# Optimization experiments

Hardware: AMD Instinct MI355X
Metric: run time of the kernel (lower is better)

The kernel has to match this reference:

```python
import jax, jax.numpy as jnp
import numpy as np

N_NODES = 50000
N_EDGES = 400000
DIMS = 32
HEADS = 6
FEAT = DIMS * HEADS  # 192
NEG_SLOPE = 0.2  # PyG GATv2Conv default


def glorot(key, shape):
    fan_in, fan_out = shape[0], shape[1]
    lim = jnp.sqrt(6.0 / (fan_in + fan_out))
    return jax.random.uniform(key, shape, jnp.float32, -lim, lim)


def setup_inputs() -> dict:
    key = jax.random.key(0)
    ks = jax.random.split(key, 10)
    x = jax.random.normal(ks[0], (N_NODES, FEAT), jnp.float32)
    edge_index = jax.random.randint(ks[1], (2, N_EDGES), 0, N_NODES, jnp.int32)
    edge_weights = jax.random.uniform(ks[2], (N_EDGES, 1), jnp.float32)
    W_l = glorot(ks[3], (FEAT, FEAT))   # lin_l: in -> heads*out
    b_l = jnp.zeros((FEAT,), jnp.float32)
    W_r = glorot(ks[4], (FEAT, FEAT))   # lin_r (share_weights=False)
    b_r = jnp.zeros((FEAT,), jnp.float32)
    W_edge = glorot(ks[5], (1, FEAT))   # lin_edge: edge_dim=1 -> heads*out, no bias
    att = glorot(ks[6], (HEADS, DIMS))  # attention vector per head
    bias = jnp.zeros((FEAT,), jnp.float32)
    return {"x": x, "edge_index": edge_index, "edge_weights": edge_weights,
            "W_l": W_l, "b_l": b_l, "W_r": W_r, "b_r": b_r,
            "W_edge": W_edge, "att": att, "bias": bias}


def gatv2_res(x, edge_index, edge_weights, W_l, b_l, W_r, b_r, W_edge, att, bias):
    N = x.shape[0]
    H, C = att.shape
    src0, dst0 = edge_index[0], edge_index[1]

    # add_self_loops with fill_value='mean': self-loop attr = mean of edge_attr over incoming edges
    cnt = jax.ops.segment_sum(jnp.ones((edge_weights.shape[0],), x.dtype), dst0, num_segments=N)
    loop_attr = jax.ops.segment_sum(edge_weights, dst0, num_segments=N) / jnp.maximum(cnt, 1.0)[:, None]
    loops = jnp.arange(N, dtype=src0.dtype)
    src = jnp.concatenate([src0, loops])
    dst = jnp.concatenate([dst0, loops])
    e_attr = jnp.concatenate([edge_weights, loop_attr], axis=0)  # [E+N, 1]

    x_l = (x @ W_l + b_l).reshape(N, H, C)  # source transform
    x_r = (x @ W_r + b_r).reshape(N, H, C)  # target transform
    e_emb = (e_attr @ W_edge).reshape(-1, H, C)

    # per-edge GATv2 score
    m = jax.nn.leaky_relu(x_l[src] + x_r[dst] + e_emb, NEG_SLOPE)  # [E+N, H, C]
    alpha = jnp.einsum('ehc,hc->eh', m, att)  # [E+N, H]

    # segment softmax over edges incident to each target node (self-loops guarantee coverage)
    amax = jax.lax.stop_gradient(jax.ops.segment_max(alpha, dst, num_segments=N))
    ex = jnp.exp(alpha - amax[dst])
    denom = jax.ops.segment_sum(ex, dst, num_segments=N)
    a = ex / denom[dst]  # [E+N, H]

    out = jax.ops.segment_sum(x_l[src] * a[..., None], dst, num_segments=N)  # [N, H, C]
    out = out.reshape(N, H * C) + bias

    # ResLayer: residual + ReLU (dropout = identity in eval mode)
    return jax.nn.relu(x + out)


def reference(x, edge_index, edge_weights, W_l, b_l, W_r, b_r, W_edge, att, bias):
    return gatv2_res(x, edge_index, edge_weights, W_l, b_l, W_r, b_r, W_edge, att, bias)
```

## Files before the change

kernel.cpp:

```cpp
#include <hip/hip_runtime.h>
#include <hip/hip_bf16.h>
#include <math.h>

#define N_NODES 50000
#define N_EDGES 400000
#define HEADS 6
#define DIMS 32
#define FEAT 192
#define NEG_SLOPE 0.2f

typedef __attribute__((ext_vector_type(8))) short short8;
typedef __attribute__((ext_vector_type(4))) float f32x4;

__device__ __forceinline__ unsigned short f2bu(float f) {
    __hip_bfloat16 h = __float2bfloat16(f);
    unsigned short u; __builtin_memcpy(&u, &h, 2); return u;
}
__device__ __forceinline__ float bu2f(unsigned short u) {
    return __uint_as_float(((unsigned)u) << 16);
}

#define XL_OFF    0
#define XR_OFF    19200000
#define WT_OFF    38400000
#define BLR_OFF   38547456
#define PAIR_OFF  38548992
#define DEG_OFF   41748992
#define SCAN_OFF  42148992
#define BSUM_OFF  42348992
#define BOFF_OFF  42350016
#define RANK_OFF  42351040
#define NB_SCAN ((N_NODES + 255) / 256)

__global__ __launch_bounds__(256) void k_count(const int* __restrict__ ei,
                                               int* __restrict__ deg,
                                               int* __restrict__ rank,
                                               const float* __restrict__ Wl,
                                               const float* __restrict__ Wr,
                                               const float* __restrict__ bl,
                                               const float* __restrict__ br,
                                               short* __restrict__ Wt,
                                               float* __restrict__ blr) {
    int e = blockIdx.x * blockDim.x + threadIdx.x;
    if (e < N_EDGES) rank[e] = atomicAdd(&deg[ei[N_EDGES + e]], 1);
    if (e < 384 * FEAT) {
        int n = e / FEAT, k = e - n * FEAT;
        float v = (n < FEAT) ? Wl[k * FEAT + n] : Wr[k * FEAT + (n - FEAT)];
        Wt[n * FEAT + k] = (short)f2bu(v);
    }
    if (e < 384) blr[e] = (e < FEAT) ? bl[e] : br[e - FEAT];
}

__global__ __launch_bounds__(256) void k_scan1(const int* __restrict__ deg,
                                               int* __restrict__ scan,
                                               int* __restrict__ bsums) {
    int t = threadIdx.x;
    int i = blockIdx.x * 256 + t;
    int v = (i < N_NODES) ? deg[i] : 0;
    __shared__ int s[256];
    s[t] = v; __syncthreads();
    for (int off = 1; off < 256; off <<= 1) {
        int u = (t >= off) ? s[t - off] : 0;
        __syncthreads();
        s[t] += u;
        __syncthreads();
    }
    if (i < N_NODES) scan[i] = s[t];
    if (t == 255) bsums[blockIdx.x] = s[255];
}

__global__ __launch_bounds__(256) void k_scan2(int* __restrict__ bsums,
                                               int* __restrict__ boffs) {
    int t = threadIdx.x;
    int v = (t < NB_SCAN) ? bsums[t] : 0;
    __shared__ int s[256];
    s[t] = v; __syncthreads();
    for (int off = 1; off < 256; off <<= 1) {
        int u = (t >= off) ? s[t - off] : 0;
        __syncthreads();
        s[t] += u;
        __syncthreads();
    }
    boffs[t] = s[t] - v;
}

__global__ __launch_bounds__(256) void k_fix(int* __restrict__ deg,
                                             const int* __restrict__ scan,
                                             const int* __restrict__ boffs) {
    int i = blockIdx.x * 256 + threadIdx.x;
    if (i < N_NODES) deg[i] = boffs[i >> 8] + scan[i] - deg[i];
}

#define SCAT_BLOCKS ((N_EDGES + 383) / 384)
#define GEMM_BLOCKS ((N_NODES + 63) / 64)
#define OSTRIDE 392
#define ASTRIDE 200
__global__ __launch_bounds__(384) void k_scatgemm(const int* __restrict__ ei,
                                                  const float* __restrict__ ew,
                                                  const int* __restrict__ deg,
                                                  const int* __restrict__ rank,
                                                  int2* __restrict__ pair,
                                                  const float* __restrict__ x,
                                                  const short* __restrict__ Wt,
                                                  const float* __restrict__ blr,
                                                  unsigned short* __restrict__ xl,
                                                  unsigned short* __restrict__ xr) {
    __shared__ unsigned short sOut[16 * OSTRIDE];
    __shared__ unsigned short sA[64 * ASTRIDE];
    if (blockIdx.x < SCAT_BLOCKS) {
        int e = blockIdx.x * 384 + threadIdx.x;
        if (e < N_EDGES) {
            int d = ei[N_EDGES + e];
            int slot = deg[d] + rank[e];
            int2 p; p.x = ei[e]; p.y = __float_as_int(ew[e]);
            pair[slot] = p;
        }
        return;
    }
    size_t row0 = (size_t)(blockIdx.x - SCAT_BLOCKS) * 64;

#pragma unroll
    for (int s = 0; s < 4; s++) {
        int q = threadIdx.x + s * 384;
        int row = q / 24, k0 = (q - row * 24) * 8;
        size_t gr = row0 + row;
        const float* ap = x + (gr < N_NODES ? gr : row0) * FEAT + k0;
        float4 v0 = *(const float4*)ap;
        float4 v1 = *(const float4*)(ap + 4);
        unsigned short tmp[8];
        tmp[0] = f2bu(v0.x); tmp[1] = f2bu(v0.y); tmp[2] = f2bu(v0.z); tmp[3] = f2bu(v0.w);
        tmp[4] = f2bu(v1.x); tmp[5] = f2bu(v1.y); tmp[6] = f2bu(v1.z); tmp[7] = f2bu(v1.w);
        int kw = (k0 >> 1) ^ ((row & 7) << 2);
        *(uint4*)&sA[row * ASTRIDE + kw * 2] = *(const uint4*)tmp;
    }
    __syncthreads();

    int wv   = threadIdx.x >> 6;
    int lane = threadIdx.x & 63;
    int m    = lane & 15;
    int kg   = lane >> 4;
    int ncol0 = wv * 64;

    f32x4 acc[4][4];
#pragma unroll
    for (int r = 0; r < 4; r++)
#pragma unroll
        for (int j = 0; j < 4; j++) acc[r][j] = (f32x4){0.f, 0.f, 0.f, 0.f};

#pragma unroll
    for (int ks = 0; ks < 6; ks++) {
        int kb = ks * 32 + kg * 8;
        int kw = (kb >> 1) ^ ((m & 7) << 2);
        short8 af0 = *(const short8*)&sA[m * ASTRIDE + kw * 2];
        short8 af1 = *(const short8*)&sA[(16 + m) * ASTRIDE + kw * 2];
        short8 af2 = *(const short8*)&sA[(32 + m) * ASTRIDE + kw * 2];
        short8 af3 = *(const short8*)&sA[(48 + m) * ASTRIDE + kw * 2];
        const short* wp = Wt + (size_t)(ncol0 + m) * FEAT + kb;
#pragma unroll
        for (int j = 0; j < 4; j++) {
            short8 b = *(const short8*)(wp + j * 16 * FEAT);
            acc[0][j] = __builtin_amdgcn_mfma_f32_16x16x32_bf16(af0, b, acc[0][j], 0, 0, 0);
            acc[1][j] = __builtin_amdgcn_mfma_f32_16x16x32_bf16(af1, b, acc[1][j], 0, 0, 0);
            acc[2][j] = __builtin_amdgcn_mfma_f32_16x16x32_bf16(af2, b, acc[2][j], 0, 0, 0);
            acc[3][j] = __builtin_amdgcn_mfma_f32_16x16x32_bf16(af3, b, acc[3][j], 0, 0, 0);
        }
    }

#pragma unroll
    for (int pass = 0; pass < 4; pass++) {
        if (pass) __syncthreads();
#pragma unroll
        for (int t4 = 0; t4 < 4; t4++) {
            int cc = ncol0 + t4 * 16 + m;
            float bv = blr[cc];
#pragma unroll
            for (int r = 0; r < 4; r++) {
                sOut[(kg * 4 + r) * OSTRIDE + cc] = f2bu(acc[pass][t4][r] + bv);
            }
        }
        __syncthreads();
        for (int q = threadIdx.x; q < 768; q += 384) {
            int row = q / 48, p = q - row * 48;
            size_t gr = row0 + pass * 16 + row;
            if (gr < N_NODES) {
                uint4 v = *(const uint4*)&sOut[row * OSTRIDE + p * 8];
                if (p < 24) *(uint4*)(xl + gr * FEAT + p * 8) = v;
                else        *(uint4*)(xr + gr * FEAT + (p - 24) * 8) = v;
            }
        }
    }
}

#define NPB 8
#define CEDGE 32
#define RS 100
#define APAD 36
__global__ __launch_bounds__(192) void k_node(const float* __restrict__ x,
                                              const float* __restrict__ bias,
                                              const float* __restrict__ att,
                                              const float* __restrict__ We,
                                              const int* __restrict__ scan,
                                              const int* __restrict__ boffs,
                                              const int2* __restrict__ pair,
                                              const unsigned short* __restrict__ xl,
                                              const unsigned short* __restrict__ xr,
                                              float* __restrict__ out) {
    __shared__ __align__(16) unsigned int sXL[CEDGE * RS];
    __shared__ __align__(16) unsigned int sXR[NPB * RS];
    __shared__ float sEx[CEDGE * HEADS];
    __shared__ float sExS[NPB * HEADS];
    __shared__ int   sSrc[2][CEDGE];
    __shared__ float sW[2][CEDGE];
    __shared__ int   sDst[2][CEDGE];
    __shared__ int   sStart[NPB + 1];
    __shared__ __align__(16) float sAttP[HEADS * APAD];
    __shared__ __align__(16) float sWeP[HEADS * APAD];
    __shared__ float sDen[NPB * HEADS];
    __shared__ float sWsm[NPB];

    int t = threadIdx.x;
    int h = t >> 5;
    int n0 = blockIdx.x * NPB;

    int gbase = boffs[n0 >> 8] + ((n0 & 255) ? scan[n0 - 1] : 0);
    int n8 = n0 + NPB;
    int gend = (n8 >= N_NODES) ? N_EDGES
             : (boffs[n8 >> 8] + ((n8 & 255) ? scan[n8 - 1] : 0));
    int etot = gend - gbase;
    int c0 = min(etot, CEDGE);

    if (t < c0) { int2 p = pair[gbase + t]; sSrc[0][t] = p.x; sW[0][t] = __int_as_float(p.y); }

    for (int q = t; q < HEADS * APAD; q += 192) {
        int hh = q / APAD, c = q - hh * APAD;
        if (c < 32) { sAttP[q] = att[hh * 32 + c]; sWeP[q] = We[hh * 32 + c]; }
    }
    if (t <= NPB) {
        int n = n0 + t;
        int st;
        if (n >= N_NODES) st = N_EDGES;
        else {
            int b = n >> 8;
            st = boffs[b] + ((n & 255) ? scan[n - 1] : 0);
        }
        sStart[t] = st;
    }
    if (t < NPB) {
        int n = n0 + t;
        int a = boffs[n >> 8] + ((n & 255) ? scan[n - 1] : 0);
        int n1 = n + 1;
        int b = (n1 >= N_NODES) ? N_EDGES
              : (boffs[n1 >> 8] + ((n1 & 255) ? scan[n1 - 1] : 0));
        int lo = a - gbase; if (lo < 0) lo = 0;
        int hi = b - gbase; if (hi > c0) hi = c0;
        for (int q = lo; q < hi; q++) sDst[0][q] = t;
    }
    {
        int nn = t / 24, p = t - nn * 24;
        *(uint4*)&sXR[nn * RS + p * 4] = ((const uint4*)(xr + (size_t)(n0 + nn) * FEAT))[p];
    }
    __syncthreads();

    float acc[NPB];
#pragma unroll
    for (int nn = 0; nn < NPB; nn++) acc[nn] = 0.f;
    float redR = 0.f;
    int nnD = t / HEADS, hhD = t - nnD * HEADS;

    int nch = (etot + CEDGE - 1) / CEDGE;
    for (int ci = 0; ci < nch; ci++) {
        int i0 = ci * CEDGE;
        int c  = min(etot - i0, CEDGE);
        int cn = min(etot - i0 - CEDGE, CEDGE);
        int cb = ci & 1, nb = cb ^ 1;

        {
            int nld = c * 24;
#pragma unroll
            for (int s = 0; s < 4; s++) {
                int q = t + s * 192;
                if (q < nld) {
                    int i = q / 24, p = q - i * 24;
                    *(uint4*)&sXL[i * RS + p * 4] =
                        *(const uint4*)(xl + (size_t)sSrc[cb][i] * FEAT + p * 8);
                }
            }
        }
        int2 P;
        if (t < cn) P = pair[gbase + i0 + CEDGE + t];
        if (t < NPB && cn > 0) {
            int lo = sStart[t] - gbase - i0 - CEDGE;     if (lo < 0) lo = 0;
            int hi = sStart[t + 1] - gbase - i0 - CEDGE; if (hi > cn) hi = cn;
            for (int q = lo; q < hi; q++) sDst[nb][q] = t;
        }
        __syncthreads();

        if (t < c * HEADS) {
            int i = t / HEADS, hh = t - i * HEADS;
            int nn = sDst[cb][i];
            float w = sW[cb][i];
            const uint4* pa = (const uint4*)&sXL[i * RS + hh * 16];
            const uint4* pb = (const uint4*)&sXR[nn * RS + hh * 16];
            float alpha0 = 0.f, alpha1 = 0.f;
#pragma unroll
            for (int g = 0; g < 4; g++) {
                uint4 a4 = pa[g];
                uint4 b4 = pb[g];
                float4 we0 = *(const float4*)&sWeP[hh * APAD + g * 8];
                float4 we1 = *(const float4*)&sWeP[hh * APAD + g * 8 + 4];
                float4 at0 = *(const float4*)&sAttP[hh * APAD + g * 8];
                float4 at1 = *(const float4*)&sAttP[hh * APAD + g * 8 + 4];
                float wec[8] = {we0.x, we0.y, we0.z, we0.w, we1.x, we1.y, we1.z, we1.w};
                float atc[8] = {at0.x, at0.y, at0.z, at0.w, at1.x, at1.y, at1.z, at1.w};
                unsigned aw[4] = {a4.x, a4.y, a4.z, a4.w};
                unsigned bw[4] = {b4.x, b4.y, b4.z, b4.w};
#pragma unroll
                for (int q = 0; q < 4; q++) {
                    float m0 = bu2f((unsigned short)aw[q]) + bu2f((unsigned short)bw[q]) + w * wec[q * 2];
                    m0 = fmaxf(m0, NEG_SLOPE * m0);
                    alpha0 += m0 * atc[q * 2];
                    float m1 = bu2f((unsigned short)(aw[q] >> 16)) + bu2f((unsigned short)(bw[q] >> 16)) + w * wec[q * 2 + 1];
                    m1 = fmaxf(m1, NEG_SLOPE * m1);
                    alpha1 += m1 * atc[q * 2 + 1];
                }
            }
            sEx[t] = __expf(alpha0 + alpha1);
        }
        if (t < cn) { sSrc[nb][t] = P.x; sW[nb][t] = __int_as_float(P.y); }
        __syncthreads();

        {
            int cw = t >> 1;
#pragma unroll
            for (int nn = 0; nn < NPB; nn++) {
                int lo = sStart[nn] - gbase - i0;     if (lo < 0) lo = 0;
                int hi = sStart[nn + 1] - gbase - i0; if (hi > c) hi = c;
                for (int i = lo; i < hi; i++) {
                    float ex = sEx[i * HEADS + h];
                    unsigned u = sXL[i * RS + cw];
                    unsigned short v = (t & 1) ? (unsigned short)(u >> 16) : (unsigned short)u;
                    acc[nn] += ex * bu2f(v);
                }
            }
            if (t < NPB * HEADS) {
                int lo = sStart[nnD] - gbase - i0;     if (lo < 0) lo = 0;
                int hi = sStart[nnD + 1] - gbase - i0; if (hi > c) hi = c;
                for (int i = lo; i < hi; i++) redR += sEx[i * HEADS + hhD];
            } else if (t < NPB * HEADS + NPB) {
                int nw = t - NPB * HEADS;
                int lo = sStart[nw] - gbase - i0;     if (lo < 0) lo = 0;
                int hi = sStart[nw + 1] - gbase - i0; if (hi > c) hi = c;
                for (int i = lo; i < hi; i++) redR += sW[cb][i];
            }
        }
        __syncthreads();
    }

    if (t < NPB * HEADS) sDen[t] = redR;
    else if (t < NPB * HEADS + NPB) sWsm[t - NPB * HEADS] = redR;
    __syncthreads();

    if (t < NPB * HEADS) {
        int nn = nnD, hh = hhD;
        int dg = sStart[nn + 1] - sStart[nn];
        float w = sWsm[nn] / fmaxf((float)dg, 1.0f);
        const uint4* pa = (const uint4*)(xl + (size_t)(n0 + nn) * FEAT + hh * 32);
        const uint4* pb = (const uint4*)&sXR[nn * RS + hh * 16];
        float alpha0 = 0.f, alpha1 = 0.f;
#pragma unroll
        for (int g = 0; g < 4; g++) {
            uint4 a4 = pa[g];
            uint4 b4 = pb[g];
            float4 we0 = *(const float4*)&sWeP[hh * APAD + g * 8];
            float4 we1 = *(const float4*)&sWeP[hh * APAD + g * 8 + 4];
            float4 at0 = *(const float4*)&sAttP[hh * APAD + g * 8];
            float4 at1 = *(const float4*)&sAttP[hh * APAD + g * 8 + 4];
            float wec[8] = {we0.x, we0.y, we0.z, we0.w, we1.x, we1.y, we1.z, we1.w};
            float atc[8] = {at0.x, at0.y, at0.z, at0.w, at1.x, at1.y, at1.z, at1.w};
            unsigned aw[4] = {a4.x, a4.y, a4.z, a4.w};
            unsigned bw[4] = {b4.x, b4.y, b4.z, b4.w};
#pragma unroll
            for (int q = 0; q < 4; q++) {
                float m0 = bu2f((unsigned short)aw[q]) + bu2f((unsigned short)bw[q]) + w * wec[q * 2];
                m0 = fmaxf(m0, NEG_SLOPE * m0);
                alpha0 += m0 * atc[q * 2];
                float m1 = bu2f((unsigned short)(aw[q] >> 16)) + bu2f((unsigned short)(bw[q] >> 16)) + w * wec[q * 2 + 1];
                m1 = fmaxf(m1, NEG_SLOPE * m1);
                alpha1 += m1 * atc[q * 2 + 1];
            }
        }
        sExS[t] = __expf(alpha0 + alpha1);
    }
    __syncthreads();

    {
        float bj = bias[t];
#pragma unroll
        for (int nn = 0; nn < NPB; nn++) {
            float exS = sExS[nn * HEADS + h];
            size_t off = (size_t)(n0 + nn) * FEAT + t;
            float xsv = bu2f(xl[off]);
            float num = acc[nn] + exS * xsv;
            float dn  = sDen[nn * HEADS + h] + exS;
            float val = x[off] + bj + num / dn;
            out[off] = (val > 0.f) ? val : 0.f;
        }
    }
}

extern "C" void kernel_launch(void* const* d_in, const int* in_sizes, int n_in,
                              void* d_out, int out_size, void* d_ws, size_t ws_size,
                              hipStream_t stream) {
    const float* x    = (const float*)d_in[0];
    const int*   ei   = (const int*)d_in[1];
    const float* ew   = (const float*)d_in[2];
    const float* Wl   = (const float*)d_in[3];
    const float* bl   = (const float*)d_in[4];
    const float* Wr   = (const float*)d_in[5];
    const float* br   = (const float*)d_in[6];
    const float* We   = (const float*)d_in[7];
    const float* att  = (const float*)d_in[8];
    const float* bias = (const float*)d_in[9];
    float* out = (float*)d_out;

    char* ws = (char*)d_ws;
    unsigned short* xl = (unsigned short*)(ws + XL_OFF);
    unsigned short* xr = (unsigned short*)(ws + XR_OFF);
    short* Wt     = (short*)(ws + WT_OFF);
    float* blr    = (float*)(ws + BLR_OFF);
    int2*  pair   = (int2*)(ws + PAIR_OFF);
    int*   deg    = (int*)(ws + DEG_OFF);
    int*   scan   = (int*)(ws + SCAN_OFF);
    int*   bsums  = (int*)(ws + BSUM_OFF);
    int*   boffs  = (int*)(ws + BOFF_OFF);
    int*   rank   = (int*)(ws + RANK_OFF);

    hipMemsetAsync(ws + DEG_OFF, 0, N_NODES * sizeof(int), stream);

    k_count<<<(N_EDGES + 255) / 256, 256, 0, stream>>>(ei, deg, rank, Wl, Wr, bl, br, Wt, blr);
    k_scan1<<<NB_SCAN, 256, 0, stream>>>(deg, scan, bsums);
    k_scan2<<<1, 256, 0, stream>>>(bsums, boffs);
    k_fix<<<NB_SCAN, 256, 0, stream>>>(deg, scan, boffs);

    k_scatgemm<<<SCAT_BLOCKS + GEMM_BLOCKS, 384, 0, stream>>>(ei, ew, deg, rank, pair,
                                                              x, Wt, blr, xl, xr);

    k_node<<<N_NODES / NPB, 192, 0, stream>>>(x, bias, att, We, scan, boffs,
                                              pair, xl, xr, out);
}
```

Before: 256.5 us.

## Shrink node kernel blocks to one wavefront covering two nodes

Reworks the aggregation kernel to process 2 target nodes per block with a single 64-thread wavefront and 8-edge chunks, instead of 8 nodes per 192-thread block with 32-edge chunks. Each thread now accumulates three feature channels across heads, and the output epilogue loops over three channel slots. The aim is finer-grained load balancing and less idle time on irregular per-node edge counts. In exchange there are many more blocks, more barrier and prologue overhead per edge, and index-scan lookups repeated across more blocks.

```diff
diff --git a/kernel.cpp b/kernel.cpp
--- a/kernel.cpp
+++ b/kernel.cpp
@@ -191,27 +191,27 @@
     }
 }
 
-#define NPB 8
-#define CEDGE 32
+#define NPB 2
+#define CE 8
 #define RS 100
 #define APAD 36
-__global__ __launch_bounds__(192) void k_node(const float* __restrict__ x,
-                                              const float* __restrict__ bias,
-                                              const float* __restrict__ att,
-                                              const float* __restrict__ We,
-                                              const int* __restrict__ scan,
-                                              const int* __restrict__ boffs,
-                                              const int2* __restrict__ pair,
-                                              const unsigned short* __restrict__ xl,
-                                              const unsigned short* __restrict__ xr,
-                                              float* __restrict__ out) {
-    __shared__ __align__(16) unsigned int sXL[CEDGE * RS];
+__global__ __launch_bounds__(64) void k_node(const float* __restrict__ x,
+                                             const float* __restrict__ bias,
+                                             const float* __restrict__ att,
+                                             const float* __restrict__ We,
+                                             const int* __restrict__ scan,
+                                             const int* __restrict__ boffs,
+                                             const int2* __restrict__ pair,
+                                             const unsigned short* __restrict__ xl,
+                                             const unsigned short* __restrict__ xr,
+                                             float* __restrict__ out) {
+    __shared__ __align__(16) unsigned int sXL[CE * RS];
     __shared__ __align__(16) unsigned int sXR[NPB * RS];
-    __shared__ float sEx[CEDGE * HEADS];
+    __shared__ float sEx[CE * HEADS];
     __shared__ float sExS[NPB * HEADS];
-    __shared__ int   sSrc[2][CEDGE];
-    __shared__ float sW[2][CEDGE];
-    __shared__ int   sDst[2][CEDGE];
+    __shared__ int   sSrc[2][CE];
+    __shared__ float sW[2][CE];
+    __shared__ int   sDst[2][CE];
     __shared__ int   sStart[NPB + 1];
     __shared__ __align__(16) float sAttP[HEADS * APAD];
     __shared__ __align__(16) float sWeP[HEADS * APAD];
@@ -219,19 +219,18 @@
     __shared__ float sWsm[NPB];
 
     int t = threadIdx.x;
-    int h = t >> 5;
     int n0 = blockIdx.x * NPB;
 
     int gbase = boffs[n0 >> 8] + ((n0 & 255) ? scan[n0 - 1] : 0);
-    int n8 = n0 + NPB;
-    int gend = (n8 >= N_NODES) ? N_EDGES
-             : (boffs[n8 >> 8] + ((n8 & 255) ? scan[n8 - 1] : 0));
+    int n2 = n0 + NPB;
+    int gend = (n2 >= N_NODES) ? N_EDGES
+             : (boffs[n2 >> 8] + ((n2 & 255) ? scan[n2 - 1] : 0));
     int etot = gend - gbase;
-    int c0 = min(etot, CEDGE);
+    int c0 = min(etot, CE);
 
     if (t < c0) { int2 p = pair[gbase + t]; sSrc[0][t] = p.x; sW[0][t] = __int_as_float(p.y); }
 
-    for (int q = t; q < HEADS * APAD; q += 192) {
+    for (int q = t; q < HEADS * APAD; q += 64) {
         int hh = q / APAD, c = q - hh * APAD;
         if (c < 32) { sAttP[q] = att[hh * 32 + c]; sWeP[q] = We[hh * 32 + c]; }
     }
@@ -255,30 +254,30 @@
         int hi = b - gbase; if (hi > c0) hi = c0;
         for (int q = lo; q < hi; q++) sDst[0][q] = t;
     }
-    {
+    if (t < NPB * 24) {
         int nn = t / 24, p = t - nn * 24;
         *(uint4*)&sXR[nn * RS + p * 4] = ((const uint4*)(xr + (size_t)(n0 + nn) * FEAT))[p];
     }
     __syncthreads();
 
-    float acc[NPB];
-#pragma unroll
-    for (int nn = 0; nn < NPB; nn++) acc[nn] = 0.f;
+    float acc[NPB][3];
+#pragma unroll
+    for (int nn = 0; nn < NPB; nn++) { acc[nn][0] = 0.f; acc[nn][1] = 0.f; acc[nn][2] = 0.f; }
     float redR = 0.f;
     int nnD = t / HEADS, hhD = t - nnD * HEADS;
 
-    int nch = (etot + CEDGE - 1) / CEDGE;
+    int nch = (etot + CE - 1) / CE;
     for (int ci = 0; ci < nch; ci++) {
-        int i0 = ci * CEDGE;
-        int c  = min(etot - i0, CEDGE);
-        int cn = min(etot - i0 - CEDGE, CEDGE);
+        int i0 = ci * CE;
+        int c  = min(etot - i0, CE);
+        int cn = min(etot - i0 - CE, CE);
         int cb = ci & 1, nb = cb ^ 1;
 
         {
             int nld = c * 24;
 #pragma unroll
-            for (int s = 0; s < 4; s++) {
-                int q = t + s * 192;
+            for (int s = 0; s < 3; s++) {
+                int q = t + s * 64;
                 if (q < nld) {
                     int i = q / 24, p = q - i * 24;
                     *(uint4*)&sXL[i * RS + p * 4] =
@@ -287,10 +286,10 @@
             }
         }
         int2 P;
-        if (t < cn) P = pair[gbase + i0 + CEDGE + t];
+        if (t < cn) P = pair[gbase + i0 + CE + t];
         if (t < NPB && cn > 0) {
-            int lo = sStart[t] - gbase - i0 - CEDGE;     if (lo < 0) lo = 0;
-            int hi = sStart[t + 1] - gbase - i0 - CEDGE; if (hi > cn) hi = cn;
+            int lo = sStart[t] - gbase - i0 - CE;     if (lo < 0) lo = 0;
+            int hi = sStart[t + 1] - gbase - i0 - CE; if (hi > cn) hi = cn;
             for (int q = lo; q < hi; q++) sDst[nb][q] = t;
         }
         __syncthreads();
@@ -330,16 +329,24 @@
         __syncthreads();
 
         {
-            int cw = t >> 1;
+            int cwb = t >> 1;
+            int hb  = t >> 5;
 #pragma unroll
             for (int nn = 0; nn < NPB; nn++) {
                 int lo = sStart[nn] - gbase - i0;     if (lo < 0) lo = 0;
                 int hi = sStart[nn + 1] - gbase - i0; if (hi > c) hi = c;
                 for (int i = lo; i < hi; i++) {
-                    float ex = sEx[i * HEADS + h];
-                    unsigned u = sXL[i * RS + cw];
-                    unsigned short v = (t & 1) ? (unsigned short)(u >> 16) : (unsigned short)u;
-                    acc[nn] += ex * bu2f(v);
+                    const unsigned int* row = &sXL[i * RS];
+                    float e0 = sEx[i * HEADS + hb];
+                    float e1 = sEx[i * HEADS + 2 + hb];
+                    float e2 = sEx[i * HEADS + 4 + hb];
+                    unsigned u0 = row[cwb], u1 = row[cwb + 32], u2 = row[cwb + 64];
+                    unsigned short v0 = (t & 1) ? (unsigned short)(u0 >> 16) : (unsigned short)u0;
+                    unsigned short v1 = (t & 1) ? (unsigned short)(u1 >> 16) : (unsigned short)u1;
+                    unsigned short v2 = (t & 1) ? (unsigned short)(u2 >> 16) : (unsigned short)u2;
+                    acc[nn][0] += e0 * bu2f(v0);
+                    acc[nn][1] += e1 * bu2f(v1);
+                    acc[nn][2] += e2 * bu2f(v2);
                 }
             }
             if (t < NPB * HEADS) {
@@ -393,15 +400,18 @@
     }
     __syncthreads();
 
-    {
-        float bj = bias[t];
+#pragma unroll
+    for (int s = 0; s < 3; s++) {
+        int ch = t + s * 64;
+        float bj = bias[ch];
+        int hh = ch >> 5;
 #pragma unroll
         for (int nn = 0; nn < NPB; nn++) {
-            float exS = sExS[nn * HEADS + h];
-            size_t off = (size_t)(n0 + nn) * FEAT + t;
+            float exS = sExS[nn * HEADS + hh];
+            size_t off = (size_t)(n0 + nn) * FEAT + ch;
             float xsv = bu2f(xl[off]);
-            float num = acc[nn] + exS * xsv;
-            float dn  = sDen[nn * HEADS + h] + exS;
+            float num = acc[nn][s] + exS * xsv;
+            float dn  = sDen[nn * HEADS + hh] + exS;
             float val = x[off] + bj + num / dn;
             out[off] = (val > 0.f) ? val : 0.f;
         }
@@ -445,6 +455,6 @@
     k_scatgemm<<<SCAT_BLOCKS + GEMM_BLOCKS, 384, 0, stream>>>(ei, ew, deg, rank, pair,
                                                               x, Wt, blr, xl, xr);
 
-    k_node<<<N_NODES / NPB, 192, 0, stream>>>(x, bias, att, We, scan, boffs,
-                                              pair, xl, xr, out);
-}
+    k_node<<<N_NODES / NPB, 64, 0, stream>>>(x, bias, att, We, scan, boffs,
+                                             pair, xl, xr, out);
+}
```

After: 253.5 us. No clear change (-1.2%).
